# Performance work log

Hardware: AMD Instinct MI355X
Metric: run time of the kernel (lower is better)

The kernel has to match this reference:

```python
import jax, jax.numpy as jnp
import numpy as np

DIM = 512
NUM_HEADS = 8
HEAD_SIZE = 64
INNER = NUM_HEADS * HEAD_SIZE  # 512


def setup_inputs() -> dict:
    key = jax.random.key(0)
    k1, k2, k3, k4, k5 = jax.random.split(key, 5)
    x = jax.random.normal(k1, (2, 4096, DIM), dtype=jnp.float32)
    # Linear params stored as [in, out] for y = x @ W + b (same math as torch Linear)
    w_qkv = jax.random.normal(k2, (DIM, INNER * 3), dtype=jnp.float32) * (1.0 / np.sqrt(DIM))
    b_qkv = jax.random.normal(k3, (INNER * 3,), dtype=jnp.float32) * 0.01
    w_out = jax.random.normal(k4, (INNER, DIM), dtype=jnp.float32) * (1.0 / np.sqrt(INNER))
    b_out = jax.random.normal(k5, (DIM,), dtype=jnp.float32) * 0.01
    return {"x": x, "w_qkv": w_qkv, "b_qkv": b_qkv, "w_out": w_out, "b_out": b_out}


def reference(x, w_qkv, b_qkv, w_out, b_out):
    b, n, _ = x.shape
    qkv = x @ w_qkv + b_qkv                      # [b, n, 3*inner]
    q, k, v = jnp.split(qkv, 3, axis=-1)          # each [b, n, inner]

    def heads(t):  # 'b n (h d) -> b h n d'
        return t.reshape(b, n, NUM_HEADS, HEAD_SIZE).transpose(0, 2, 1, 3)

    q, k, v = heads(q), heads(k), heads(v)
    scores = jnp.einsum('bhnd,bhmd->bhnm', q, k) / jnp.sqrt(jnp.float32(HEAD_SIZE))
    probs = jax.nn.softmax(scores, axis=-1)       # dropout is identity in eval
    out = jnp.einsum('bhnm,bhmd->bhnd', probs, v)
    out = out.transpose(0, 2, 1, 3).reshape(b, n, INNER)  # 'b h n d -> b n (h d)'
    return out @ w_out + b_out
```

## Files before the change

### kernel.cpp

```cpp
#include <hip/hip_runtime.h>

typedef __bf16 bf16;
typedef __bf16 bf16x8 __attribute__((ext_vector_type(8)));
typedef float f32x4 __attribute__((ext_vector_type(4)));
typedef unsigned u32x4 __attribute__((ext_vector_type(4)));

#define MFMA16(a, b, c) __builtin_amdgcn_mfma_f32_16x16x32_bf16((a), (b), (c), 0, 0, 0)

static __device__ __forceinline__ bf16x8 ldg8(const bf16* p) {
  return *(const bf16x8*)p;
}
static __device__ __forceinline__ unsigned cvt_pk_bf16(float lo, float hi) {
  unsigned d;
  asm("v_cvt_pk_bf16_f32 %0, %1, %2" : "=v"(d) : "v"(lo), "v"(hi));
  return d;
}
static __device__ __forceinline__ void pl32_swap(unsigned& a, unsigned& b) {
  asm("v_permlane32_swap_b32 %0, %1" : "+v"(a), "+v"(b));
}
static __device__ __forceinline__ void pl16_swap(unsigned& a, unsigned& b) {
  asm("v_permlane16_swap_b32 %0, %1" : "+v"(a), "+v"(b));
}


__global__ __launch_bounds__(256) void pack_weights(const float* __restrict__ Wqkv,
                                                    const float* __restrict__ Wout,
                                                    bf16* __restrict__ Wp1,
                                                    bf16* __restrict__ Wp2) {
  __shared__ float tile[32 * 129];
  int kc = blockIdx.x, nt = blockIdx.y;
  const float* W;
  bf16* dst;
  int N, ntl;
  if (nt < 12) {
    W = Wqkv; N = 1536; ntl = nt;
    dst = Wp1 + ((size_t)ntl * 16 + kc) * 4096;
  } else {
    W = Wout; N = 512; ntl = nt - 12;
    dst = Wp2 + ((size_t)ntl * 16 + kc) * 4096;
  }
  int row = threadIdx.x >> 3;
  int c0 = (threadIdx.x & 7) * 16;
  const float* src = W + (size_t)(kc * 32 + row) * N + ntl * 128 + c0;
#pragma unroll
  for (int i = 0; i < 4; i++) {
    float4 v = *(const float4*)(src + i * 4);
    tile[row * 129 + c0 + i * 4 + 0] = v.x;
    tile[row * 129 + c0 + i * 4 + 1] = v.y;
    tile[row * 129 + c0 + i * 4 + 2] = v.z;
    tile[row * 129 + c0 + i * 4 + 3] = v.w;
  }
  __syncthreads();
#pragma unroll
  for (int half = 0; half < 2; half++) {
    int U = threadIdx.x + half * 256;
    int kchunk = U >> 7, n = U & 127;
    bf16x8 o;
#pragma unroll
    for (int j = 0; j < 8; j++) o[j] = (bf16)tile[(kchunk * 8 + j) * 129 + n];
    *(bf16x8*)&dst[U * 8] = o;
  }
}

__global__ __launch_bounds__(256, 3) void qkv_gemm(const float* __restrict__ x,
                                                   const bf16* __restrict__ Wp1,
                                                   const float* __restrict__ bqkv,
                                                   bf16* __restrict__ Q,
                                                   bf16* __restrict__ Kh,
                                                   bf16* __restrict__ Vt) {
  int mt = blockIdx.x, nt = blockIdx.y;
  int tid = threadIdx.x;
  int wave = tid >> 6, lane = tid & 63;
  int l16 = lane & 15, quad = lane >> 4;
  int wr = wave >> 1, wc = wave & 1;

  __shared__ __align__(16) bf16 SM[9216];

  int r = tid >> 1, khalf = tid & 1;
  const float* xs = x + (size_t)(mt * 128 + r) * 512 + khalf * 16;
  const bf16* Bt = Wp1 + (size_t)nt * 16 * 4096;
  int lwA0 = ((khalf * 2 + 0) * 128 + r) * 8;
  int lwA1 = ((khalf * 2 + 1) * 128 + r) * 8;

  float4 fa0 = *(const float4*)(xs + 0);
  float4 fa1 = *(const float4*)(xs + 4);
  float4 fa2 = *(const float4*)(xs + 8);
  float4 fa3 = *(const float4*)(xs + 12);

  f32x4 acc[4][4] = {};
#pragma unroll 2
  for (int kc = 0; kc < 16; kc++) {
    bf16* A = SM + (kc & 1) * 4096;
    u32x4 pk0 = {cvt_pk_bf16(fa0.x, fa0.y), cvt_pk_bf16(fa0.z, fa0.w),
                 cvt_pk_bf16(fa1.x, fa1.y), cvt_pk_bf16(fa1.z, fa1.w)};
    u32x4 pk1 = {cvt_pk_bf16(fa2.x, fa2.y), cvt_pk_bf16(fa2.z, fa2.w),
                 cvt_pk_bf16(fa3.x, fa3.y), cvt_pk_bf16(fa3.z, fa3.w)};
    *(bf16x8*)&A[lwA0] = __builtin_bit_cast(bf16x8, pk0);
    *(bf16x8*)&A[lwA1] = __builtin_bit_cast(bf16x8, pk1);
    __syncthreads();
    if (kc < 15) {
      const float* xn = xs + (kc + 1) * 32;
      fa0 = *(const float4*)(xn + 0);
      fa1 = *(const float4*)(xn + 4);
      fa2 = *(const float4*)(xn + 8);
      fa3 = *(const float4*)(xn + 12);
    }
    bf16x8 af[4], bfr[4];
#pragma unroll
    for (int fi = 0; fi < 4; fi++)
      af[fi] = *(const bf16x8*)&A[(quad * 128 + wr * 64 + fi * 16 + l16) * 8];
    const bf16* Bk = Bt + kc * 4096;
#pragma unroll
    for (int fj = 0; fj < 4; fj++)
      bfr[fj] = ldg8(Bk + (quad * 128 + wc * 64 + fj * 16 + l16) * 8);
    __builtin_amdgcn_s_setprio(1);
#pragma unroll
    for (int fi = 0; fi < 4; fi++)
#pragma unroll
      for (int fj = 0; fj < 4; fj++)
        acc[fi][fj] = MFMA16(af[fi], bfr[fj], acc[fi][fj]);
    __builtin_amdgcn_s_setprio(0);
  }

  __syncthreads();
  const int TS = 72;
  int b = mt >> 5;

  if (nt < 8) {
    bool isQ = nt < 4;
    bf16* dstb = isQ ? Q : Kh;
    int hb = isQ ? nt * 2 : (nt - 4) * 2;
#pragma unroll
    for (int ph = 0; ph < 2; ph++) {
      if (wc == ph) {
#pragma unroll
        for (int fj = 0; fj < 4; fj++) {
          float bias = bqkv[nt * 128 + wc * 64 + fj * 16 + l16];
#pragma unroll
          for (int fi = 0; fi < 4; fi++)
#pragma unroll
            for (int rr = 0; rr < 4; rr++) {
              float v = acc[fi][fj][rr] + bias;
              if (isQ) v *= 0.18033688f;
              SM[(wr * 64 + fi * 16 + quad * 4 + rr) * TS + fj * 16 + l16] =
                  (bf16)v;
            }
        }
      }
      __syncthreads();
      int bh = b * 8 + hb + ph;
      bf16* dh = dstb + (size_t)bh * 4096 * 64 + (size_t)((mt & 31) * 128) * 64;
#pragma unroll
      for (int i = 0; i < 4; i++) {
        int U = tid + i * 256;
        int mr = U >> 3, oct = U & 7;
        bf16x8 v = ldg8(&SM[mr * TS + oct * 8]);
        *(bf16x8*)&dh[(size_t)mr * 64 + oct * 8] = v;
      }
      __syncthreads();
    }
  } else {
    int h0 = (nt - 8) * 2;
#pragma unroll
    for (int ph = 0; ph < 2; ph++) {
      if (wr == ph) {
#pragma unroll
        for (int fj = 0; fj < 4; fj++) {
          float bias = bqkv[nt * 128 + wc * 64 + fj * 16 + l16];
          int cp = wc * 64 + fj * 16 + l16;
#pragma unroll
          for (int fi = 0; fi < 4; fi++)
#pragma unroll
            for (int rr = 0; rr < 4; rr++)
              SM[cp * TS + fi * 16 + quad * 4 + rr] =
                  (bf16)(acc[fi][fj][rr] + bias);
        }
      }
      __syncthreads();
      int nb = (mt & 31) * 2 + ph;
#pragma unroll
      for (int i = 0; i < 4; i++) {
        int U = tid + i * 256;
        int cp = U >> 3, oct = U & 7;
        int h = h0 + (cp >> 6), d = cp & 63;
        int bh = b * 8 + h;
        bf16x8 v = ldg8(&SM[cp * TS + oct * 8]);
        *(bf16x8*)&Vt[(((size_t)bh * 64 + nb) * 64 + d) * 64 + oct * 8] = v;
      }
      __syncthreads();
    }
  }
}

__global__ __launch_bounds__(256, 4) void flash_partial(const bf16* __restrict__ Q,
                                                        const bf16* __restrict__ K,
                                                        const bf16* __restrict__ Vt,
                                                        bf16* __restrict__ Opart,
                                                        float* __restrict__ Lpart) {
  int strip = blockIdx.x, bh = blockIdx.y, half = blockIdx.z;
  int tid = threadIdx.x;
  int wave = tid >> 6, lane = tid & 63;
  int l16 = lane & 15, quad = lane >> 4;

  const bf16* Qh = Q + (size_t)bh * 4096 * 64;
  const bf16* Kg = K + ((size_t)bh * 4096 + half * 2048) * 64;
  const bf16* Vg = Vt + (size_t)bh * 64 * 4096 + (size_t)half * 2048 * 64;

  __shared__ __align__(16) bf16 Klds[2][4096];
  __shared__ __align__(16) bf16 Vlds[2][4096];

  int qbase = strip * 128 + wave * 32;
  bf16x8 aq[2][2];
#pragma unroll
  for (int mt = 0; mt < 2; mt++) {
    const bf16* qr = Qh + (size_t)(qbase + mt * 16 + l16) * 64;
    aq[mt][0] = ldg8(qr + quad * 8);
    aq[mt][1] = ldg8(qr + 32 + quad * 8);
  }

  bf16x8 ones;
#pragma unroll
  for (int i = 0; i < 8; i++) ones[i] = (bf16)1.0f;

  f32x4 o[2][4] = {};
  f32x4 acc_l[2] = {};

  int e0 = tid * 8, e1 = (256 + tid) * 8;
  int r0 = e0 >> 6, r1 = e1 >> 6;
  int u0 = r0 * 8 + (((e0 & 63) >> 3) ^ (r0 & 7));
  int u1 = r1 * 8 + (((e1 & 63) >> 3) ^ (r1 & 7));

  bf16x8 kp0 = ldg8(Kg + e0), kp1 = ldg8(Kg + e1);
  bf16x8 vp0 = ldg8(Vg + e0), vp1 = ldg8(Vg + e1);

#pragma unroll 2
  for (int t = 0; t < 32; t++) {
    int cur = t & 1;
    bf16* kl = Klds[cur];
    bf16* vl = Vlds[cur];
    *(bf16x8*)&kl[u0 * 8] = kp0;
    *(bf16x8*)&kl[u1 * 8] = kp1;
    *(bf16x8*)&vl[u0 * 8] = vp0;
    *(bf16x8*)&vl[u1 * 8] = vp1;
    __syncthreads();

    if (t < 31) {
      const bf16* kg = Kg + (size_t)(t + 1) * 4096;
      const bf16* vg = Vg + (size_t)(t + 1) * 4096;
      kp0 = ldg8(kg + e0);
      kp1 = ldg8(kg + e1);
      vp0 = ldg8(vg + e0);
      vp1 = ldg8(vg + e1);
    }

#pragma unroll
    for (int h2 = 0; h2 < 2; h2++) {
      f32x4 s[2][2] = {};
      __builtin_amdgcn_s_setprio(1);
#pragma unroll
      for (int c2 = 0; c2 < 2; c2++) {
        int n = h2 * 32 + c2 * 16 + l16;
        bf16x8 k0 = *(const bf16x8*)&kl[(n * 8 + (quad ^ (n & 7))) * 8];
        bf16x8 k1 = *(const bf16x8*)&kl[(n * 8 + ((4 + quad) ^ (n & 7))) * 8];
#pragma unroll
        for (int mt = 0; mt < 2; mt++) {
          s[mt][c2] = MFMA16(k0, aq[mt][0], s[mt][c2]);
          s[mt][c2] = MFMA16(k1, aq[mt][1], s[mt][c2]);
        }
      }
      __builtin_amdgcn_s_setprio(0);

      bf16x8 pa[2];
#pragma unroll
      for (int mt = 0; mt < 2; mt++) {
        unsigned ue[2], wo[2];
#pragma unroll
        for (int c2 = 0; c2 < 2; c2++) {
          float p0 = __builtin_amdgcn_exp2f(s[mt][c2][0]);
          float p1 = __builtin_amdgcn_exp2f(s[mt][c2][1]);
          float p2 = __builtin_amdgcn_exp2f(s[mt][c2][2]);
          float p3 = __builtin_amdgcn_exp2f(s[mt][c2][3]);
          ue[c2] = cvt_pk_bf16(p0, p1);
          wo[c2] = cvt_pk_bf16(p2, p3);
        }
        pl32_swap(ue[0], ue[1]);
        pl16_swap(ue[0], ue[1]);
        pl32_swap(wo[0], wo[1]);
        pl16_swap(wo[0], wo[1]);
        u32x4 pk = {ue[0], wo[0], ue[1], wo[1]};
        pa[mt] = __builtin_bit_cast(bf16x8, pk);
      }

      __builtin_amdgcn_s_setprio(1);
      acc_l[0] = MFMA16(pa[0], ones, acc_l[0]);
      acc_l[1] = MFMA16(pa[1], ones, acc_l[1]);
#pragma unroll
      for (int ct = 0; ct < 4; ct++) {
        int d = ct * 16 + l16;
        bf16x8 bv = *(const bf16x8*)&vl[(d * 8 + ((h2 * 4 + quad) ^ (d & 7))) * 8];
        o[0][ct] = MFMA16(pa[0], bv, o[0][ct]);
        o[1][ct] = MFMA16(pa[1], bv, o[1][ct]);
      }
      __builtin_amdgcn_s_setprio(0);
    }
  }

  size_t ub = ((size_t)half * 16 + bh) * 32 + strip;
  bf16* op = Opart + ub * 8192;
#pragma unroll
  for (int mt = 0; mt < 2; mt++) {
#pragma unroll
    for (int ct = 0; ct < 4; ct++)
#pragma unroll
      for (int r = 0; r < 4; r++)
        op[(wave * 32 + mt * 16 + quad * 4 + r) * 64 + ct * 16 + l16] =
            (bf16)o[mt][ct][r];
    if (l16 == 0) {
#pragma unroll
      for (int r = 0; r < 4; r++)
        Lpart[ub * 128 + wave * 32 + mt * 16 + quad * 4 + r] = acc_l[mt][r];
    }
  }
}

__global__ __launch_bounds__(256) void flash_combine(const bf16* __restrict__ Opart,
                                                     const float* __restrict__ Lpart,
                                                     bf16* __restrict__ Ap) {
  int mt = blockIdx.x, kc = blockIdx.y;
  int b = mt >> 5, strip = mt & 31;
  int h = kc >> 1, d0 = (kc & 1) * 32;
  int bh = b * 8 + h;
  size_t u0 = (size_t)bh * 32 + strip;
  size_t u1 = ((size_t)16 + bh) * 32 + strip;
  bf16* dst = Ap + ((size_t)mt * 16 + kc) * 4096;
#pragma unroll
  for (int hf = 0; hf < 2; hf++) {
    int U = threadIdx.x + hf * 256;
    int kchunk = U >> 7, r = U & 127;
    bf16x8 o0 = ldg8(&Opart[u0 * 8192 + r * 64 + d0 + kchunk * 8]);
    bf16x8 o1 = ldg8(&Opart[u1 * 8192 + r * 64 + d0 + kchunk * 8]);
    float ls = Lpart[u0 * 128 + r] + Lpart[u1 * 128 + r];
    float rl = 1.0f / ls;
    bf16x8 ov;
#pragma unroll
    for (int j = 0; j < 8; j++)
      ov[j] = (bf16)(((float)o0[j] + (float)o1[j]) * rl);
    *(bf16x8*)&dst[U * 8] = ov;
  }
}

__global__ __launch_bounds__(256, 4) void out_gemm(const bf16* __restrict__ Ap,
                                                   const bf16* __restrict__ Wp2,
                                                   const float* __restrict__ bout,
                                                   float* __restrict__ Out) {
  int mt = blockIdx.x, nt = blockIdx.y;
  int tid = threadIdx.x;
  int wave = tid >> 6, lane = tid & 63;
  int l16 = lane & 15, quad = lane >> 4;
  int mt128 = mt >> 1, mhalf = mt & 1;

  __shared__ __align__(16) bf16 SM[2][2048];

  const bf16* At = Ap + (size_t)mt128 * 16 * 4096;
  const bf16* Bt = Wp2 + (size_t)nt * 16 * 4096;
  int guni = (tid >> 6) * 128 + mhalf * 64 + (tid & 63);

  bf16x8 pa = ldg8(At + guni * 8);
  f32x4 acc[4][2] = {};
#pragma unroll 2
  for (int kc = 0; kc < 16; kc++) {
    bf16* A = SM[kc & 1];
    *(bf16x8*)&A[tid * 8] = pa;
    __syncthreads();
    if (kc < 15) pa = ldg8(At + (kc + 1) * 4096 + guni * 8);
    bf16x8 af[4], bfr[2];
#pragma unroll
    for (int fi = 0; fi < 4; fi++)
      af[fi] = *(const bf16x8*)&A[(quad * 64 + fi * 16 + l16) * 8];
    const bf16* Bk = Bt + kc * 4096;
#pragma unroll
    for (int fj = 0; fj < 2; fj++)
      bfr[fj] = ldg8(Bk + (quad * 128 + wave * 32 + fj * 16 + l16) * 8);
    __builtin_amdgcn_s_setprio(1);
#pragma unroll
    for (int fi = 0; fi < 4; fi++)
#pragma unroll
      for (int fj = 0; fj < 2; fj++)
        acc[fi][fj] = MFMA16(af[fi], bfr[fj], acc[fi][fj]);
    __builtin_amdgcn_s_setprio(0);
  }

#pragma unroll
  for (int fj = 0; fj < 2; fj++) {
    int c = nt * 128 + wave * 32 + fj * 16 + l16;
    float bias = bout[c];
#pragma unroll
    for (int fi = 0; fi < 4; fi++) {
#pragma unroll
      for (int r = 0; r < 4; r++) {
        int m = mt * 64 + fi * 16 + quad * 4 + r;
        Out[(size_t)m * 512 + c] = acc[fi][fj][r] + bias;
      }
    }
  }
}

extern "C" void kernel_launch(void* const* d_in, const int* in_sizes, int n_in,
                              void* d_out, int out_size, void* d_ws,
                              size_t ws_size, hipStream_t stream) {
  const float* x = (const float*)d_in[0];
  const float* w_qkv = (const float*)d_in[1];
  const float* b_qkv = (const float*)d_in[2];
  const float* w_out = (const float*)d_in[3];
  const float* b_out = (const float*)d_in[4];
  float* out = (float*)d_out;

  char* ws = (char*)d_ws;
  bf16* Q = (bf16*)(ws + 0);
  bf16* K = (bf16*)(ws + 8388608);
  bf16* Vt = (bf16*)(ws + 16777216);
  bf16* Wp2 = (bf16*)(ws + 25165824);
  bf16* Opart = (bf16*)(ws + 25690112);
  float* Lpart = (float*)(ws + 42467328);
  bf16* Wp1 = (bf16*)(ws + 42991616);
  bf16* Ap = (bf16*)(ws + 0);

  pack_weights<<<dim3(16, 16), 256, 0, stream>>>(w_qkv, w_out, Wp1, Wp2);
  qkv_gemm<<<dim3(64, 12), 256, 0, stream>>>(x, Wp1, b_qkv, Q, K, Vt);
  flash_partial<<<dim3(32, 16, 2), 256, 0, stream>>>(Q, K, Vt, Opart, Lpart);
  flash_combine<<<dim3(64, 16), 256, 0, stream>>>(Opart, Lpart, Ap);
  out_gemm<<<dim3(128, 4), 256, 0, stream>>>(Ap, Wp2, b_out, out);
}
```

Before: 191.2 us.

## Pre-pack x to bf16 in prep kernel and fuse flash combine into out GEMM

The weight-packing kernel now also converts x to bf16 in the tiled layout, so the QKV GEMM loads bf16 tiles directly instead of converting fp32 each K step. The separate flash_combine kernel is removed, and out_gemm now reads both split-KV partial outputs and their row sums, combining and normalizing them while staging A into shared memory. This removes one launch and the Ap round trip through global memory. In exchange, out_gemm reads twice the partial data and does extra conversion work per tile, and each of the 4 N-tile blocks repeats that combine for the same rows.

After: 192.8 us. No clear change (+0.8%).

```diff
diff --git a/kernel.cpp b/kernel.cpp
--- a/kernel.cpp
+++ b/kernel.cpp
@@ -23,46 +23,68 @@
 }
 
 
-__global__ __launch_bounds__(256) void pack_weights(const float* __restrict__ Wqkv,
-                                                    const float* __restrict__ Wout,
-                                                    bf16* __restrict__ Wp1,
-                                                    bf16* __restrict__ Wp2) {
+__global__ __launch_bounds__(256) void prep(const float* __restrict__ Wqkv,
+                                            const float* __restrict__ Wout,
+                                            const float* __restrict__ x,
+                                            bf16* __restrict__ Wp1,
+                                            bf16* __restrict__ Wp2,
+                                            bf16* __restrict__ Xp) {
   __shared__ float tile[32 * 129];
-  int kc = blockIdx.x, nt = blockIdx.y;
-  const float* W;
-  bf16* dst;
-  int N, ntl;
-  if (nt < 12) {
-    W = Wqkv; N = 1536; ntl = nt;
-    dst = Wp1 + ((size_t)ntl * 16 + kc) * 4096;
+  if (blockIdx.x < 16) {
+    int kc = blockIdx.x, nt = blockIdx.y;
+    const float* W;
+    bf16* dst;
+    int N, ntl;
+    if (nt < 12) {
+      W = Wqkv; N = 1536; ntl = nt;
+      dst = Wp1 + ((size_t)ntl * 16 + kc) * 4096;
+    } else {
+      W = Wout; N = 512; ntl = nt - 12;
+      dst = Wp2 + ((size_t)ntl * 16 + kc) * 4096;
+    }
+    int row = threadIdx.x >> 3;
+    int c0 = (threadIdx.x & 7) * 16;
+    const float* src = W + (size_t)(kc * 32 + row) * N + ntl * 128 + c0;
+#pragma unroll
+    for (int i = 0; i < 4; i++) {
+      float4 v = *(const float4*)(src + i * 4);
+      tile[row * 129 + c0 + i * 4 + 0] = v.x;
+      tile[row * 129 + c0 + i * 4 + 1] = v.y;
+      tile[row * 129 + c0 + i * 4 + 2] = v.z;
+      tile[row * 129 + c0 + i * 4 + 3] = v.w;
+    }
+    __syncthreads();
+#pragma unroll
+    for (int half = 0; half < 2; half++) {
+      int U = threadIdx.x + half * 256;
+      int kchunk = U >> 7, n = U & 127;
+      bf16x8 o;
+#pragma unroll
+      for (int j = 0; j < 8; j++) o[j] = (bf16)tile[(kchunk * 8 + j) * 129 + n];
+      *(bf16x8*)&dst[U * 8] = o;
+    }
   } else {
-    W = Wout; N = 512; ntl = nt - 12;
-    dst = Wp2 + ((size_t)ntl * 16 + kc) * 4096;
-  }
-  int row = threadIdx.x >> 3;
-  int c0 = (threadIdx.x & 7) * 16;
-  const float* src = W + (size_t)(kc * 32 + row) * N + ntl * 128 + c0;
-#pragma unroll
-  for (int i = 0; i < 4; i++) {
-    float4 v = *(const float4*)(src + i * 4);
-    tile[row * 129 + c0 + i * 4 + 0] = v.x;
-    tile[row * 129 + c0 + i * 4 + 1] = v.y;
-    tile[row * 129 + c0 + i * 4 + 2] = v.z;
-    tile[row * 129 + c0 + i * 4 + 3] = v.w;
-  }
-  __syncthreads();
-#pragma unroll
-  for (int half = 0; half < 2; half++) {
-    int U = threadIdx.x + half * 256;
-    int kchunk = U >> 7, n = U & 127;
-    bf16x8 o;
-#pragma unroll
-    for (int j = 0; j < 8; j++) o[j] = (bf16)tile[(kchunk * 8 + j) * 129 + n];
-    *(bf16x8*)&dst[U * 8] = o;
-  }
-}
-
-__global__ __launch_bounds__(256, 3) void qkv_gemm(const float* __restrict__ x,
+    int mt = blockIdx.x - 16, kc = blockIdx.y;
+    int r = threadIdx.x >> 1;
+    int khalf = threadIdx.x & 1;
+    const float* src = x + (size_t)(mt * 128 + r) * 512 + kc * 32 + khalf * 16;
+    float4 v0 = *(const float4*)(src + 0);
+    float4 v1 = *(const float4*)(src + 4);
+    float4 v2 = *(const float4*)(src + 8);
+    float4 v3 = *(const float4*)(src + 12);
+    bf16* dt = Xp + ((size_t)mt * 16 + kc) * 4096;
+    bf16x8 a, b;
+    a[0] = (bf16)v0.x; a[1] = (bf16)v0.y; a[2] = (bf16)v0.z; a[3] = (bf16)v0.w;
+    a[4] = (bf16)v1.x; a[5] = (bf16)v1.y; a[6] = (bf16)v1.z; a[7] = (bf16)v1.w;
+    b[0] = (bf16)v2.x; b[1] = (bf16)v2.y; b[2] = (bf16)v2.z; b[3] = (bf16)v2.w;
+    b[4] = (bf16)v3.x; b[5] = (bf16)v3.y; b[6] = (bf16)v3.z; b[7] = (bf16)v3.w;
+    int kc0 = khalf * 2;
+    *(bf16x8*)&dt[(kc0 + 0) * 1024 + r * 8] = a;
+    *(bf16x8*)&dt[(kc0 + 1) * 1024 + r * 8] = b;
+  }
+}
+
+__global__ __launch_bounds__(256, 3) void qkv_gemm(const bf16* __restrict__ Xp,
                                                    const bf16* __restrict__ Wp1,
                                                    const float* __restrict__ bqkv,
                                                    bf16* __restrict__ Q,
@@ -76,34 +98,23 @@
 
   __shared__ __align__(16) bf16 SM[9216];
 
-  int r = tid >> 1, khalf = tid & 1;
-  const float* xs = x + (size_t)(mt * 128 + r) * 512 + khalf * 16;
+  const bf16* At = Xp + (size_t)mt * 16 * 4096;
   const bf16* Bt = Wp1 + (size_t)nt * 16 * 4096;
-  int lwA0 = ((khalf * 2 + 0) * 128 + r) * 8;
-  int lwA1 = ((khalf * 2 + 1) * 128 + r) * 8;
-
-  float4 fa0 = *(const float4*)(xs + 0);
-  float4 fa1 = *(const float4*)(xs + 4);
-  float4 fa2 = *(const float4*)(xs + 8);
-  float4 fa3 = *(const float4*)(xs + 12);
+
+  bf16x8 pa0 = ldg8(At + tid * 8);
+  bf16x8 pa1 = ldg8(At + 2048 + tid * 8);
 
   f32x4 acc[4][4] = {};
 #pragma unroll 2
   for (int kc = 0; kc < 16; kc++) {
     bf16* A = SM + (kc & 1) * 4096;
-    u32x4 pk0 = {cvt_pk_bf16(fa0.x, fa0.y), cvt_pk_bf16(fa0.z, fa0.w),
-                 cvt_pk_bf16(fa1.x, fa1.y), cvt_pk_bf16(fa1.z, fa1.w)};
-    u32x4 pk1 = {cvt_pk_bf16(fa2.x, fa2.y), cvt_pk_bf16(fa2.z, fa2.w),
-                 cvt_pk_bf16(fa3.x, fa3.y), cvt_pk_bf16(fa3.z, fa3.w)};
-    *(bf16x8*)&A[lwA0] = __builtin_bit_cast(bf16x8, pk0);
-    *(bf16x8*)&A[lwA1] = __builtin_bit_cast(bf16x8, pk1);
+    *(bf16x8*)&A[tid * 8] = pa0;
+    *(bf16x8*)&A[2048 + tid * 8] = pa1;
     __syncthreads();
     if (kc < 15) {
-      const float* xn = xs + (kc + 1) * 32;
-      fa0 = *(const float4*)(xn + 0);
-      fa1 = *(const float4*)(xn + 4);
-      fa2 = *(const float4*)(xn + 8);
-      fa3 = *(const float4*)(xn + 12);
+      const bf16* an = At + (kc + 1) * 4096;
+      pa0 = ldg8(an + tid * 8);
+      pa1 = ldg8(an + 2048 + tid * 8);
     }
     bf16x8 af[4], bfr[4];
 #pragma unroll
@@ -323,33 +334,8 @@
   }
 }
 
-__global__ __launch_bounds__(256) void flash_combine(const bf16* __restrict__ Opart,
-                                                     const float* __restrict__ Lpart,
-                                                     bf16* __restrict__ Ap) {
-  int mt = blockIdx.x, kc = blockIdx.y;
-  int b = mt >> 5, strip = mt & 31;
-  int h = kc >> 1, d0 = (kc & 1) * 32;
-  int bh = b * 8 + h;
-  size_t u0 = (size_t)bh * 32 + strip;
-  size_t u1 = ((size_t)16 + bh) * 32 + strip;
-  bf16* dst = Ap + ((size_t)mt * 16 + kc) * 4096;
-#pragma unroll
-  for (int hf = 0; hf < 2; hf++) {
-    int U = threadIdx.x + hf * 256;
-    int kchunk = U >> 7, r = U & 127;
-    bf16x8 o0 = ldg8(&Opart[u0 * 8192 + r * 64 + d0 + kchunk * 8]);
-    bf16x8 o1 = ldg8(&Opart[u1 * 8192 + r * 64 + d0 + kchunk * 8]);
-    float ls = Lpart[u0 * 128 + r] + Lpart[u1 * 128 + r];
-    float rl = 1.0f / ls;
-    bf16x8 ov;
-#pragma unroll
-    for (int j = 0; j < 8; j++)
-      ov[j] = (bf16)(((float)o0[j] + (float)o1[j]) * rl);
-    *(bf16x8*)&dst[U * 8] = ov;
-  }
-}
-
-__global__ __launch_bounds__(256, 4) void out_gemm(const bf16* __restrict__ Ap,
+__global__ __launch_bounds__(256, 4) void out_gemm(const bf16* __restrict__ Opart,
+                                                   const float* __restrict__ Lpart,
                                                    const bf16* __restrict__ Wp2,
                                                    const float* __restrict__ bout,
                                                    float* __restrict__ Out) {
@@ -358,21 +344,51 @@
   int wave = tid >> 6, lane = tid & 63;
   int l16 = lane & 15, quad = lane >> 4;
   int mt128 = mt >> 1, mhalf = mt & 1;
+  int b = mt128 >> 5, strip = mt128 & 31;
+  int r = mhalf * 64 + lane;
 
   __shared__ __align__(16) bf16 SM[2][2048];
 
-  const bf16* At = Ap + (size_t)mt128 * 16 * 4096;
   const bf16* Bt = Wp2 + (size_t)nt * 16 * 4096;
-  int guni = (tid >> 6) * 128 + mhalf * 64 + (tid & 63);
-
-  bf16x8 pa = ldg8(At + guni * 8);
+
+  bf16x8 po0, po1;
+  float pls;
+  {
+    int h = 0, d0 = 0;
+    int bh = b * 8 + h;
+    size_t s0 = ((size_t)bh * 32 + strip);
+    size_t s1 = (((size_t)16 + bh) * 32 + strip);
+    po0 = ldg8(&Opart[s0 * 8192 + r * 64 + d0 + wave * 8]);
+    po1 = ldg8(&Opart[s1 * 8192 + r * 64 + d0 + wave * 8]);
+    pls = Lpart[s0 * 128 + r] + Lpart[s1 * 128 + r];
+  }
+
   f32x4 acc[4][2] = {};
 #pragma unroll 2
   for (int kc = 0; kc < 16; kc++) {
     bf16* A = SM[kc & 1];
-    *(bf16x8*)&A[tid * 8] = pa;
+    float rl = 1.0f / pls;
+    u32x4 pk = {
+        cvt_pk_bf16(((float)po0[0] + (float)po1[0]) * rl,
+                    ((float)po0[1] + (float)po1[1]) * rl),
+        cvt_pk_bf16(((float)po0[2] + (float)po1[2]) * rl,
+                    ((float)po0[3] + (float)po1[3]) * rl),
+        cvt_pk_bf16(((float)po0[4] + (float)po1[4]) * rl,
+                    ((float)po0[5] + (float)po1[5]) * rl),
+        cvt_pk_bf16(((float)po0[6] + (float)po1[6]) * rl,
+                    ((float)po0[7] + (float)po1[7]) * rl)};
+    *(bf16x8*)&A[tid * 8] = __builtin_bit_cast(bf16x8, pk);
     __syncthreads();
-    if (kc < 15) pa = ldg8(At + (kc + 1) * 4096 + guni * 8);
+    if (kc < 15) {
+      int kn = kc + 1;
+      int h = kn >> 1, d0 = (kn & 1) * 32;
+      int bh = b * 8 + h;
+      size_t s0 = ((size_t)bh * 32 + strip);
+      size_t s1 = (((size_t)16 + bh) * 32 + strip);
+      po0 = ldg8(&Opart[s0 * 8192 + r * 64 + d0 + wave * 8]);
+      po1 = ldg8(&Opart[s1 * 8192 + r * 64 + d0 + wave * 8]);
+      pls = Lpart[s0 * 128 + r] + Lpart[s1 * 128 + r];
+    }
     bf16x8 af[4], bfr[2];
 #pragma unroll
     for (int fi = 0; fi < 4; fi++)
@@ -397,9 +413,9 @@
 #pragma unroll
     for (int fi = 0; fi < 4; fi++) {
 #pragma unroll
-      for (int r = 0; r < 4; r++) {
-        int m = mt * 64 + fi * 16 + quad * 4 + r;
-        Out[(size_t)m * 512 + c] = acc[fi][fj][r] + bias;
+      for (int rr = 0; rr < 4; rr++) {
+        int m = mt * 64 + fi * 16 + quad * 4 + rr;
+        Out[(size_t)m * 512 + c] = acc[fi][fj][rr] + bias;
       }
     }
   }
@@ -423,11 +439,10 @@
   bf16* Opart = (bf16*)(ws + 25690112);
   float* Lpart = (float*)(ws + 42467328);
   bf16* Wp1 = (bf16*)(ws + 42991616);
-  bf16* Ap = (bf16*)(ws + 0);
-
-  pack_weights<<<dim3(16, 16), 256, 0, stream>>>(w_qkv, w_out, Wp1, Wp2);
-  qkv_gemm<<<dim3(64, 12), 256, 0, stream>>>(x, Wp1, b_qkv, Q, K, Vt);
+  bf16* Xp = (bf16*)(ws + 44564480);
+
+  prep<<<dim3(80, 16), 256, 0, stream>>>(w_qkv, w_out, x, Wp1, Wp2, Xp);
+  qkv_gemm<<<dim3(64, 12), 256, 0, stream>>>(Xp, Wp1, b_qkv, Q, K, Vt);
   flash_partial<<<dim3(32, 16, 2), 256, 0, stream>>>(Q, K, Vt, Opart, Lpart);
-  flash_combine<<<dim3(64, 16), 256, 0, stream>>>(Opart, Lpart, Ap);
-  out_gemm<<<dim3(128, 4), 256, 0, stream>>>(Ap, Wp2, b_out, out);
-}
+  out_gemm<<<dim3(128, 4), 256, 0, stream>>>(Opart, Lpart, Wp2, b_out, out);
+}
```
